# Kernel optimization log

Measured on AMD Instinct MI355X. Metric: run time of the kernel, lower is better.

Reference implementation:

```python
import jax, jax.numpy as jnp
import numpy as np

N = 8192
IN_FEATS = 512
OUT_FEATS = 512


def setup_inputs() -> dict:
    key = jax.random.key(0)
    k_adj, k_feat, k_w = jax.random.split(key, 3)
    adj = jax.random.uniform(k_adj, (N, N), dtype=jnp.float32)
    features = jax.random.normal(k_feat, (N, IN_FEATS), dtype=jnp.float32)
    # nn.Linear(in_feats, out_feats, bias=False): weight is [out, in]; we store transposed [in, out]
    W = jax.random.normal(k_w, (IN_FEATS, OUT_FEATS), dtype=jnp.float32) / np.sqrt(IN_FEATS)
    return {"adj": adj, "features": features, "W": W}


def reference(adj, features, W):
    n = adj.shape[0]
    # adj + I (self loops)
    a = adj + jnp.eye(n, dtype=adj.dtype)
    # symmetric degree normalization D^{-1/2} A D^{-1/2}
    deg = jnp.sum(a, axis=1)  # [N]
    d_inv_sqrt = jnp.where(deg > 0, jax.lax.rsqrt(deg), 0.0)  # inf -> 0 as in torch code
    # diag(d) @ a @ diag(d) == d[:,None] * a * d[None,:] (algebraic simplification of O(N^3) diag matmuls)
    norm_adj = d_inv_sqrt[:, None] * a * d_inv_sqrt[None, :]  # [N, N]
    h = norm_adj @ features  # [N, in]
    return h @ W  # [N, out]
```

## Files before the change

kernel.cpp:

```cpp
#include <hip/hip_runtime.h>
#include <cstdint>
#include <cstddef>

#define NN 8192
#define NF 512
#define SPLITK 4

typedef __attribute__((ext_vector_type(8))) short bf16x8;
typedef __attribute__((ext_vector_type(8))) unsigned short u16x8;
typedef __attribute__((ext_vector_type(4))) float f32x4;

__device__ __forceinline__ unsigned short f2bf_bits(float f) {
  unsigned u = __builtin_bit_cast(unsigned, f);
  u += 0x7FFFu + ((u >> 16) & 1u);
  return (unsigned short)(u >> 16);
}

__device__ __forceinline__ float bf2f(unsigned short b) {
  return __builtin_bit_cast(float, (unsigned)b << 16);
}

__device__ __forceinline__ bf16x8 cvt8(float4 a, float4 b) {
  bf16x8 r;
  r[0] = (short)f2bf_bits(a.x); r[1] = (short)f2bf_bits(a.y);
  r[2] = (short)f2bf_bits(a.z); r[3] = (short)f2bf_bits(a.w);
  r[4] = (short)f2bf_bits(b.x); r[5] = (short)f2bf_bits(b.y);
  r[6] = (short)f2bf_bits(b.z); r[7] = (short)f2bf_bits(b.w);
  return r;
}

__device__ __forceinline__ void gld_lds16(const void* g, void* l) {
  __builtin_amdgcn_global_load_lds(
      (const __attribute__((address_space(1))) unsigned int*)g,
      (__attribute__((address_space(3))) unsigned int*)l, 16, 0, 0);
}

template <bool CVT>
__global__ void k_rowsum(const float* __restrict__ adj, float* __restrict__ dinv,
                         short* __restrict__ adjb) {
  const int row = blockIdx.x;
  const float4* p = (const float4*)(adj + (size_t)row * NN);
  short* ob = CVT ? (adjb + (size_t)row * NN) : nullptr;
  float s = 0.f;
#pragma unroll
  for (int j = 0; j < 8; ++j) {
    float4 v = p[j * 256 + threadIdx.x];
    s += (v.x + v.y) + (v.z + v.w);
    if (CVT) {
      ushort4 o;
      o.x = f2bf_bits(v.x); o.y = f2bf_bits(v.y);
      o.z = f2bf_bits(v.z); o.w = f2bf_bits(v.w);
      *(ushort4*)&ob[(size_t)(j * 256 + threadIdx.x) * 4] = o;
    }
  }
#pragma unroll
  for (int off = 32; off > 0; off >>= 1) s += __shfl_down(s, off, 64);
  __shared__ float red[4];
  if ((threadIdx.x & 63) == 0) red[threadIdx.x >> 6] = s;
  __syncthreads();
  if (threadIdx.x == 0) {
    float deg = red[0] + red[1] + red[2] + red[3] + 1.0f;
    dinv[row] = (deg > 0.f) ? (1.0f / sqrtf(deg)) : 0.f;
  }
}

template <bool SCALE>
__global__ void k_transpose(const float* __restrict__ src, int rows, int cols,
                            const float* __restrict__ dinv, short* __restrict__ dst) {
  __shared__ float tile[32][33];
  const int c0 = blockIdx.x * 32, r0 = blockIdx.y * 32;
  const int tx = threadIdx.x & 31, ty = threadIdx.x >> 5;
#pragma unroll
  for (int i = 0; i < 32; i += 8) {
    float v = src[(size_t)(r0 + ty + i) * cols + c0 + tx];
    if (SCALE) v *= dinv[r0 + ty + i];
    tile[ty + i][tx] = v;
  }
  __syncthreads();
#pragma unroll
  for (int i = 0; i < 32; i += 8)
    dst[(size_t)(c0 + ty + i) * rows + r0 + tx] = (short)f2bf_bits(tile[tx][ty + i]);
}

__global__ __launch_bounds__(512, 1)
void k_gemm8(const short* __restrict__ Ab, const short* __restrict__ Bt,
             int N, int K, unsigned short* __restrict__ Pout) {
  __shared__ __align__(16) short As[3][2][256 * 32];
  __shared__ __align__(16) short Bs[2][2][256 * 32];
  const int tid = threadIdx.x, lane = tid & 63, w = tid >> 6;
  const int wm = w >> 2, wn = w & 3;

  const int hid = (blockIdx.z * gridDim.y + blockIdx.y) * gridDim.x + blockIdx.x;
  const int xcd = hid & 7, rr = hid >> 3;
  const int pair = xcd * 16 + (rr >> 1);
  const int member = rr & 1;
  const int m0 = (pair & 31) * 256;
  const int n0 = member * 256;
  const int kz = pair >> 5;
  const int ksl = K / SPLITK;
  const int kbase = kz * ksl;
  const int nt = ksl >> 6;
  unsigned short* Cp = Pout + (size_t)kz * ((size_t)NN * (size_t)N);

  f32x4 acc[8][4];
#pragma unroll
  for (int m = 0; m < 8; ++m)
#pragma unroll
    for (int n = 0; n < 4; ++n) acc[m][n] = (f32x4){0.f, 0.f, 0.f, 0.f};

  const int lr = lane & 15, kg = lane >> 4;

  auto stageA = [&](int buf, int t) {
#pragma unroll
    for (int h = 0; h < 2; ++h) {
      const int kofs = kbase + (t << 6) + (h << 5) + ((lane & 3) << 3);
#pragma unroll
      for (int rnd = 0; rnd < 2; ++rnd) {
        const int rowb = (rnd << 7) + (w << 4);
        const int row = rowb + (lane >> 2);
        gld_lds16(Ab + (size_t)(m0 + row) * K + kofs, &As[buf][h][rowb << 5]);
      }
    }
  };
  auto stageB = [&](int buf, int t) {
#pragma unroll
    for (int h = 0; h < 2; ++h) {
      const int kofs = kbase + (t << 6) + (h << 5) + ((lane & 3) << 3);
#pragma unroll
      for (int rnd = 0; rnd < 2; ++rnd) {
        const int rowb = (rnd << 7) + (w << 4);
        const int row = rowb + (lane >> 2);
        gld_lds16(Bt + (size_t)(n0 + row) * K + kofs, &Bs[buf][h][rowb << 5]);
      }
    }
  };
  auto readA = [&](int buf, int kh, bf16x8* a) {
#pragma unroll
    for (int mf = 0; mf < 8; ++mf)
      a[mf] = *(const bf16x8*)&As[buf][kh][(((wm << 7) + (mf << 4) + lr) << 5) + (kg << 3)];
  };
  auto readB2 = [&](int buf, int kh, int nh, bf16x8* b) {
#pragma unroll
    for (int i = 0; i < 2; ++i)
      b[i] = *(const bf16x8*)&Bs[buf][kh][(((wn << 6) + (((nh << 1) + i) << 4) + lr) << 5) + (kg << 3)];
  };
  auto mfma16 = [&](bf16x8* a, bf16x8* b, int nh) {
#pragma unroll
    for (int mf = 0; mf < 8; ++mf)
#pragma unroll
      for (int i = 0; i < 2; ++i)
        acc[mf][(nh << 1) + i] =
            __builtin_amdgcn_mfma_f32_16x16x32_bf16(a[mf], b[i], acc[mf][(nh << 1) + i], 0, 0, 0);
  };

  stageA(0, 0);
  stageB(0, 0);
  stageA(1, 1);

  for (int t = 0; t < nt; ++t) {
    const int ab = t % 3, bb = t & 1;
    bf16x8 a[8], b0[2], b1[2];
    if (t + 1 < nt) asm volatile("s_waitcnt vmcnt(4)" ::: "memory");
    else            asm volatile("s_waitcnt vmcnt(0)" ::: "memory");
    __builtin_amdgcn_s_barrier();
    __builtin_amdgcn_sched_barrier(0);
    readA(ab, 0, a);
    readB2(bb, 0, 0, b0);
    if (t + 1 < nt) stageB((t + 1) & 1, t + 1);
    asm volatile("s_waitcnt lgkmcnt(0)" ::: "memory");
    __builtin_amdgcn_sched_barrier(0);
    __builtin_amdgcn_s_setprio(1);
    mfma16(a, b0, 0);
    __builtin_amdgcn_s_setprio(0);
    __builtin_amdgcn_sched_barrier(0);
    readB2(bb, 0, 1, b1);
    asm volatile("s_waitcnt lgkmcnt(0)" ::: "memory");
    __builtin_amdgcn_sched_barrier(0);
    __builtin_amdgcn_s_setprio(1);
    mfma16(a, b1, 1);
    __builtin_amdgcn_s_setprio(0);
    __builtin_amdgcn_sched_barrier(0);
    readA(ab, 1, a);
    readB2(bb, 1, 0, b0);
    if (t + 2 < nt) stageA((t + 2) % 3, t + 2);
    asm volatile("s_waitcnt lgkmcnt(0)" ::: "memory");
    __builtin_amdgcn_sched_barrier(0);
    __builtin_amdgcn_s_setprio(1);
    mfma16(a, b0, 0);
    __builtin_amdgcn_s_setprio(0);
    __builtin_amdgcn_sched_barrier(0);
    readB2(bb, 1, 1, b1);
    asm volatile("s_waitcnt lgkmcnt(0)" ::: "memory");
    __builtin_amdgcn_sched_barrier(0);
    __builtin_amdgcn_s_setprio(1);
    mfma16(a, b1, 1);
    __builtin_amdgcn_s_setprio(0);
    __builtin_amdgcn_sched_barrier(0);
  }

  const int cl = lane & 15, rg = lane >> 4;
#pragma unroll
  for (int mf = 0; mf < 8; ++mf)
#pragma unroll
    for (int nf = 0; nf < 4; ++nf)
#pragma unroll
      for (int j = 0; j < 4; ++j) {
        const int gi = m0 + (wm << 7) + (mf << 4) + (rg << 2) + j;
        const int gn = n0 + (wn << 6) + (nf << 4) + cl;
        Cp[(size_t)gi * N + gn] = f2bf_bits(acc[mf][nf][j]);
      }
}

__global__ void k_reduce(const unsigned short* __restrict__ P, const float* __restrict__ dinv,
                         const float* __restrict__ feat, short* __restrict__ Hb) {
  const size_t idx = ((size_t)blockIdx.x * 256 + threadIdx.x) * 8;
  const int i = (int)(idx >> 9);
  const size_t stride = (size_t)NN * NF;
  float s[8] = {0.f, 0.f, 0.f, 0.f, 0.f, 0.f, 0.f, 0.f};
#pragma unroll
  for (int kz = 0; kz < SPLITK; ++kz) {
    u16x8 v = *(const u16x8*)&P[kz * stride + idx];
#pragma unroll
    for (int j = 0; j < 8; ++j) s[j] += bf2f(v[j]);
  }
  const float d = dinv[i], d2 = d * d;
  float4 f0 = *(const float4*)&feat[idx];
  float4 f1 = *(const float4*)&feat[idx + 4];
  u16x8 o;
  o[0] = f2bf_bits(d * s[0] + d2 * f0.x);
  o[1] = f2bf_bits(d * s[1] + d2 * f0.y);
  o[2] = f2bf_bits(d * s[2] + d2 * f0.z);
  o[3] = f2bf_bits(d * s[3] + d2 * f0.w);
  o[4] = f2bf_bits(d * s[4] + d2 * f1.x);
  o[5] = f2bf_bits(d * s[5] + d2 * f1.y);
  o[6] = f2bf_bits(d * s[6] + d2 * f1.z);
  o[7] = f2bf_bits(d * s[7] + d2 * f1.w);
  *(u16x8*)&Hb[idx] = o;
}

template <bool A_BF16, bool GCN_EPI>
__global__ __launch_bounds__(512, 2)
void k_gemm2(const void* __restrict__ Ap, const short* __restrict__ Bt,
             int N, int K,
             const float* __restrict__ dinv, const float* __restrict__ feat,
             void* __restrict__ Cp) {
  __shared__ __align__(16) short As[4][128 * 64];
  __shared__ __align__(16) short Bs[4][128 * 64];
  const int tid = threadIdx.x;
  const int lane = tid & 63;
  const int w = tid >> 6;
  const int wm = (w >> 1) & 1, wn = w & 1, kk = w >> 2;

  const int bid = blockIdx.y * gridDim.x + blockIdx.x;
  const int nb = gridDim.x * gridDim.y;
  const int sbid = ((nb & 7) == 0) ? ((bid & 7) * (nb >> 3) + (bid >> 3)) : bid;
  const int n0 = (sbid % gridDim.x) * 128;
  const int m0 = (sbid / gridDim.x) * 128;
  const int nt = K >> 6;

  f32x4 acc[4][4];
#pragma unroll
  for (int m = 0; m < 4; ++m)
#pragma unroll
    for (int n = 0; n < 4; ++n) acc[m][n] = (f32x4){0.f, 0.f, 0.f, 0.f};

  const int lr = lane & 15, kg = lane >> 4;
  const int lc = (kk << 2) + kg;

  auto stage_b = [&](int buf, int t) {
    const int kofs = t << 6;
#pragma unroll
    for (int q = 0; q < 2; ++q) {
      const int rblk = (w << 4) + (q << 3);
      const int r = rblk + (lane >> 3);
      const int sc = (lane & 7) ^ (r & 7);
      gld_lds16(Bt + (size_t)(n0 + r) * K + kofs + (sc << 3), &Bs[buf][rblk << 6]);
    }
  };
  auto stage_a = [&](int buf, int t) {
    const int kofs = t << 6;
    const short* Ab = (const short*)Ap;
#pragma unroll
    for (int q = 0; q < 2; ++q) {
      const int rblk = (w << 4) + (q << 3);
      const int r = rblk + (lane >> 3);
      const int sc = (lane & 7) ^ (r & 7);
      gld_lds16(Ab + (size_t)(m0 + r) * K + kofs + (sc << 3), &As[buf][rblk << 6]);
    }
  };
  auto stage_a_f32 = [&](int buf, int t) {
    const int kofs = t << 6;
    const float* Af = (const float*)Ap;
    const int r = tid >> 2;
    const int c0 = (tid & 3) << 4;
    const float* s = Af + (size_t)(m0 + r) * K + kofs + c0;
    float4 x0 = ((const float4*)s)[0], x1 = ((const float4*)s)[1];
    float4 x2 = ((const float4*)s)[2], x3 = ((const float4*)s)[3];
    const int cc = (tid & 3) << 1;
    *(bf16x8*)&As[buf][(r << 6) + ((cc ^ (r & 7)) << 3)]       = cvt8(x0, x1);
    *(bf16x8*)&As[buf][(r << 6) + (((cc + 1) ^ (r & 7)) << 3)] = cvt8(x2, x3);
  };
  auto read_a = [&](int buf, bf16x8* a) {
#pragma unroll
    for (int m = 0; m < 4; ++m) {
      const int r = (wm << 6) + (m << 4) + lr;
      a[m] = *(const bf16x8*)&As[buf][(r << 6) + ((lc ^ (r & 7)) << 3)];
    }
  };
  auto read_b2 = [&](int buf, int nh, bf16x8* b) {
#pragma unroll
    for (int i = 0; i < 2; ++i) {
      const int r = (wn << 6) + (((nh << 1) + i) << 4) + lr;
      b[i] = *(const bf16x8*)&Bs[buf][(r << 6) + ((lc ^ (r & 7)) << 3)];
    }
  };
  auto mfma8 = [&](bf16x8* a, bf16x8* b, int nh) {
#pragma unroll
    for (int m = 0; m < 4; ++m)
#pragma unroll
      for (int i = 0; i < 2; ++i)
        acc[m][(nh << 1) + i] =
            __builtin_amdgcn_mfma_f32_16x16x32_bf16(a[m], b[i], acc[m][(nh << 1) + i], 0, 0, 0);
  };

  if constexpr (A_BF16) {
    stage_a(0, 0); stage_b(0, 0);
    stage_a(1, 1); stage_b(1, 1);
    asm volatile("s_waitcnt vmcnt(4)" ::: "memory");
    __builtin_amdgcn_s_barrier();
    __builtin_amdgcn_sched_barrier(0);
    for (int t = 0; t < nt; ++t) {
      const int cur = t & 3;
      const bool more = (t + 2 < nt);
      bf16x8 a[4], b0[2], b1[2];
      read_a(cur, a);
      read_b2(cur, 0, b0);
      if (more) stage_a((t + 2) & 3, t + 2);
      __builtin_amdgcn_s_barrier();
      asm volatile("s_waitcnt lgkmcnt(0)" ::: "memory");
      __builtin_amdgcn_sched_barrier(0);
      __builtin_amdgcn_s_setprio(1);
      mfma8(a, b0, 0);
      __builtin_amdgcn_s_setprio(0);
      __builtin_amdgcn_sched_barrier(0);
      read_b2(cur, 1, b1);
      if (more) stage_b((t + 2) & 3, t + 2);
      asm volatile("s_waitcnt lgkmcnt(0)" ::: "memory");
      __builtin_amdgcn_sched_barrier(0);
      __builtin_amdgcn_s_setprio(1);
      mfma8(a, b1, 1);
      __builtin_amdgcn_s_setprio(0);
      __builtin_amdgcn_sched_barrier(0);
      if (more)            asm volatile("s_waitcnt vmcnt(4)" ::: "memory");
      else if (t + 1 < nt) asm volatile("s_waitcnt vmcnt(0)" ::: "memory");
      __builtin_amdgcn_s_barrier();
      __builtin_amdgcn_sched_barrier(0);
    }
  } else {
    stage_a_f32(0, 0); stage_b(0, 0);
    stage_a_f32(1, 1); stage_b(1, 1);
    __syncthreads();
    for (int t = 0; t < nt; ++t) {
      const int cur = t & 3;
      if (t + 2 < nt) { stage_a_f32((t + 2) & 3, t + 2); stage_b((t + 2) & 3, t + 2); }
      bf16x8 a[4], b0[2], b1[2];
      read_a(cur, a); read_b2(cur, 0, b0); read_b2(cur, 1, b1);
      __builtin_amdgcn_s_setprio(1);
      mfma8(a, b0, 0); mfma8(a, b1, 1);
      __builtin_amdgcn_s_setprio(0);
      __syncthreads();
    }
  }

  __syncthreads();
  float* red = (float*)&As[0][0];
  if (w >= 4) {
    float* my = red + ((w - 4) << 12);
#pragma unroll
    for (int m = 0; m < 4; ++m)
#pragma unroll
      for (int n = 0; n < 4; ++n)
        *(f32x4*)&my[(((m << 2) + n) << 8) + (lane << 2)] = acc[m][n];
  }
  __syncthreads();
  if (w < 4) {
    float* my = red + (w << 12);
#pragma unroll
    for (int m = 0; m < 4; ++m)
#pragma unroll
      for (int n = 0; n < 4; ++n)
        acc[m][n] += *(const f32x4*)&my[(((m << 2) + n) << 8) + (lane << 2)];
    const int cl = lane & 15, rg = lane >> 4;
#pragma unroll
    for (int m = 0; m < 4; ++m)
#pragma unroll
      for (int n = 0; n < 4; ++n)
#pragma unroll
        for (int j = 0; j < 4; ++j) {
          const int gi = m0 + (wm << 6) + (m << 4) + (rg << 2) + j;
          const int gn = n0 + (wn << 6) + (n << 4) + cl;
          const float v = acc[m][n][j];
          if constexpr (GCN_EPI) {
            const float d = dinv[gi];
            const float hv = d * v + d * d * feat[(size_t)gi * NF + gn];
            ((unsigned short*)Cp)[(size_t)gi * N + gn] = f2bf_bits(hv);
          } else {
            ((float*)Cp)[(size_t)gi * N + gn] = v;
          }
        }
  }
}

extern "C" void kernel_launch(void* const* d_in, const int* in_sizes, int n_in,
                              void* d_out, int out_size, void* d_ws, size_t ws_size,
                              hipStream_t stream) {
  const float* adj  = (const float*)d_in[0];
  const float* feat = (const float*)d_in[1];
  const float* W    = (const float*)d_in[2];

  char* ws = (char*)d_ws;
  float* dinv = (float*)ws;
  short* FbT  = (short*)(ws + 32768);
  short* WbT  = (short*)(ws + 32768 + 8388608);
  short* Hb   = (short*)(ws + 32768 + 8388608 + 524288);
  short* adjb = (short*)(ws + 32768 + 8388608 + 524288 + 8388608);
  unsigned short* part = (unsigned short*)(ws + 32768 + 8388608 + 524288 + 8388608 + 134217728);
  float* out  = (float*)d_out;
  const size_t need = (size_t)32768 + 8388608 + 524288 + 8388608 + 134217728 +
                      (size_t)SPLITK * NN * NF * 2;
  const bool big_ws = ws_size >= need;

  if (big_ws) {
    k_rowsum<true><<<NN, 256, 0, stream>>>(adj, dinv, adjb);
  } else {
    k_rowsum<false><<<NN, 256, 0, stream>>>(adj, dinv, nullptr);
  }
  k_transpose<true ><<<dim3(NF / 32, NN / 32), 256, 0, stream>>>(feat, NN, NF, dinv, FbT);
  k_transpose<false><<<dim3(NF / 32, NF / 32), 256, 0, stream>>>(W, NF, NF, nullptr, WbT);

  if (big_ws) {
    k_gemm8<<<dim3(NF / 256, NN / 256, SPLITK), 512, 0, stream>>>(adjb, FbT, NF, NN, part);
    k_reduce<<<(NN * NF) / (256 * 8), 256, 0, stream>>>(part, dinv, feat, Hb);
  } else {
    k_gemm2<false, true><<<dim3(NF / 128, NN / 128), 512, 0, stream>>>(
        adj, FbT, NF, NN, dinv, feat, Hb);
  }
  k_gemm2<true, false><<<dim3(NF / 128, NN / 128), 512, 0, stream>>>(
      Hb, WbT, NF, NF, nullptr, nullptr, out);
}
```

Baseline: 169.9 us.

## Split global-to-LDS staging into halves interleaved with MFMA phases and barriers

```diff
diff --git a/kernel.cpp b/kernel.cpp
--- a/kernel.cpp
+++ b/kernel.cpp
@@ -110,28 +110,22 @@
 
   const int lr = lane & 15, kg = lane >> 4;
 
-  auto stageA = [&](int buf, int t) {
-#pragma unroll
-    for (int h = 0; h < 2; ++h) {
-      const int kofs = kbase + (t << 6) + (h << 5) + ((lane & 3) << 3);
-#pragma unroll
-      for (int rnd = 0; rnd < 2; ++rnd) {
-        const int rowb = (rnd << 7) + (w << 4);
-        const int row = rowb + (lane >> 2);
-        gld_lds16(Ab + (size_t)(m0 + row) * K + kofs, &As[buf][h][rowb << 5]);
-      }
-    }
-  };
-  auto stageB = [&](int buf, int t) {
-#pragma unroll
-    for (int h = 0; h < 2; ++h) {
-      const int kofs = kbase + (t << 6) + (h << 5) + ((lane & 3) << 3);
-#pragma unroll
-      for (int rnd = 0; rnd < 2; ++rnd) {
-        const int rowb = (rnd << 7) + (w << 4);
-        const int row = rowb + (lane >> 2);
-        gld_lds16(Bt + (size_t)(n0 + row) * K + kofs, &Bs[buf][h][rowb << 5]);
-      }
+  auto stageA_h = [&](int buf, int t, int h) {
+    const int kofs = kbase + (t << 6) + (h << 5) + ((lane & 3) << 3);
+#pragma unroll
+    for (int rnd = 0; rnd < 2; ++rnd) {
+      const int rowb = (rnd << 7) + (w << 4);
+      const int row = rowb + (lane >> 2);
+      gld_lds16(Ab + (size_t)(m0 + row) * K + kofs, &As[buf][h][rowb << 5]);
+    }
+  };
+  auto stageB_h = [&](int buf, int t, int h) {
+    const int kofs = kbase + (t << 6) + (h << 5) + ((lane & 3) << 3);
+#pragma unroll
+    for (int rnd = 0; rnd < 2; ++rnd) {
+      const int rowb = (rnd << 7) + (w << 4);
+      const int row = rowb + (lane >> 2);
+      gld_lds16(Bt + (size_t)(n0 + row) * K + kofs, &Bs[buf][h][rowb << 5]);
     }
   };
   auto readA = [&](int buf, int kh, bf16x8* a) {
@@ -153,48 +147,62 @@
             __builtin_amdgcn_mfma_f32_16x16x32_bf16(a[mf], b[i], acc[mf][(nh << 1) + i], 0, 0, 0);
   };
 
-  stageA(0, 0);
-  stageB(0, 0);
-  stageA(1, 1);
+  stageA_h(0, 0, 0); stageA_h(0, 0, 1);
+  stageB_h(0, 0, 0); stageB_h(0, 0, 1);
+  stageA_h(1, 1, 0); stageA_h(1, 1, 1);
+  asm volatile("s_waitcnt vmcnt(4)" ::: "memory");
+  __builtin_amdgcn_s_barrier();
+  __builtin_amdgcn_sched_barrier(0);
 
   for (int t = 0; t < nt; ++t) {
     const int ab = t % 3, bb = t & 1;
+    const int abn = (t + 2) % 3, bbn = (t + 1) & 1;
+    const bool sA = (t + 2 < nt), sB = (t + 1 < nt);
     bf16x8 a[8], b0[2], b1[2];
-    if (t + 1 < nt) asm volatile("s_waitcnt vmcnt(4)" ::: "memory");
-    else            asm volatile("s_waitcnt vmcnt(0)" ::: "memory");
-    __builtin_amdgcn_s_barrier();
-    __builtin_amdgcn_sched_barrier(0);
     readA(ab, 0, a);
     readB2(bb, 0, 0, b0);
-    if (t + 1 < nt) stageB((t + 1) & 1, t + 1);
+    if (sB) stageB_h(bbn, t + 1, 0);
+    __builtin_amdgcn_s_barrier();
     asm volatile("s_waitcnt lgkmcnt(0)" ::: "memory");
     __builtin_amdgcn_sched_barrier(0);
     __builtin_amdgcn_s_setprio(1);
     mfma16(a, b0, 0);
     __builtin_amdgcn_s_setprio(0);
     __builtin_amdgcn_sched_barrier(0);
+    __builtin_amdgcn_s_barrier();
     readB2(bb, 0, 1, b1);
+    if (sB) stageB_h(bbn, t + 1, 1);
+    __builtin_amdgcn_s_barrier();
     asm volatile("s_waitcnt lgkmcnt(0)" ::: "memory");
     __builtin_amdgcn_sched_barrier(0);
     __builtin_amdgcn_s_setprio(1);
     mfma16(a, b1, 1);
     __builtin_amdgcn_s_setprio(0);
     __builtin_amdgcn_sched_barrier(0);
+    __builtin_amdgcn_s_barrier();
     readA(ab, 1, a);
     readB2(bb, 1, 0, b0);
-    if (t + 2 < nt) stageA((t + 2) % 3, t + 2);
+    if (sA) stageA_h(abn, t + 2, 0);
+    __builtin_amdgcn_s_barrier();
     asm volatile("s_waitcnt lgkmcnt(0)" ::: "memory");
     __builtin_amdgcn_sched_barrier(0);
     __builtin_amdgcn_s_setprio(1);
     mfma16(a, b0, 0);
     __builtin_amdgcn_s_setprio(0);
     __builtin_amdgcn_sched_barrier(0);
+    __builtin_amdgcn_s_barrier();
     readB2(bb, 1, 1, b1);
+    if (sA) stageA_h(abn, t + 2, 1);
+    __builtin_amdgcn_s_barrier();
     asm volatile("s_waitcnt lgkmcnt(0)" ::: "memory");
     __builtin_amdgcn_sched_barrier(0);
     __builtin_amdgcn_s_setprio(1);
     mfma16(a, b1, 1);
     __builtin_amdgcn_s_setprio(0);
+    __builtin_amdgcn_sched_barrier(0);
+    if (sA)      asm volatile("s_waitcnt vmcnt(4)" ::: "memory");
+    else if (sB) asm volatile("s_waitcnt vmcnt(0)" ::: "memory");
+    __builtin_amdgcn_s_barrier();
     __builtin_amdgcn_sched_barrier(0);
   }
 
```

After: 181.0 us. 1.07x slower.
